# Optimization experiments

Measured on AMD Instinct MI355X. Metric: run time of the kernel, lower is better.

The kernel has to match this reference:

```python
import jax, jax.numpy as jnp
import numpy as np

B, L, D_BERT, D_PROJ, N_SPANS, HIDDEN, EXTRA = 128, 512, 1024, 64, 3, 512, 17
BN_EPS = 1e-5


def setup_inputs() -> dict:
    key = jax.random.key(0)
    ks = jax.random.split(key, 20)
    inp = {
        "bert_outputs": jax.random.normal(ks[0], (B, L, D_BERT), jnp.float32),
        "offsets": jnp.sort(jax.random.randint(ks[1], (B, N_SPANS, 2), 0, L), axis=-1),
        "in_urls": jax.random.uniform(ks[2], (B, 3), jnp.float32),
        "other_feats": jax.random.normal(ks[3], (B, 14), jnp.float32),
        # context conv (Conv1d: out=64, in=1024, k=3)
        "conv_w": jax.random.normal(ks[4], (D_PROJ, D_BERT, 3), jnp.float32) * 0.02,
        "conv_b": jnp.zeros((D_PROJ,), jnp.float32),
        # span extractor global attention Linear(64 -> 1)
        "att_w": jax.random.normal(ks[5], (D_PROJ,), jnp.float32) * 0.1,
        "att_b": jnp.zeros((), jnp.float32),
        # BatchNorm1d(192) in eval mode (running stats)
        "bn1_g": jnp.ones((D_PROJ * 3,), jnp.float32),
        "bn1_b": jnp.zeros((D_PROJ * 3,), jnp.float32),
        "bn1_m": jax.random.normal(ks[6], (D_PROJ * 3,), jnp.float32) * 0.1,
        "bn1_v": jax.random.uniform(ks[7], (D_PROJ * 3,), jnp.float32, 0.5, 1.5),
        # Linear(192 -> 512), kaiming
        "fc_w": jax.random.normal(ks[8], (HIDDEN, D_PROJ * 3), jnp.float32) * np.sqrt(2.0 / (D_PROJ * 3)),
        "fc_b": jnp.zeros((HIDDEN,), jnp.float32),
        # BatchNorm1d(512)
        "bn2_g": jnp.ones((HIDDEN,), jnp.float32),
        "bn2_b": jnp.zeros((HIDDEN,), jnp.float32),
        "bn2_m": jax.random.normal(ks[9], (HIDDEN,), jnp.float32) * 0.1,
        "bn2_v": jax.random.uniform(ks[10], (HIDDEN,), jnp.float32, 0.5, 1.5),
        # new_last_layer Linear(512+17 -> 3)
        "last_w": jax.random.normal(ks[11], (3, HIDDEN + EXTRA), jnp.float32) * 0.05,
        "last_b": jnp.zeros((3,), jnp.float32),
    }
    return inp


def _bn_eval(x, g, b, m, v):
    return (x - m) * jax.lax.rsqrt(v + BN_EPS) * g + b


def reference(bert_outputs, offsets, in_urls, other_feats, conv_w, conv_b,
              att_w, att_b, bn1_g, bn1_b, bn1_m, bn1_v, fc_w, fc_b,
              bn2_g, bn2_b, bn2_m, bn2_v, last_w, last_b):
    # Conv1d over sequence: [B,L,Dbert] -> [B,L,64], padding preserves length
    x = jnp.transpose(bert_outputs, (0, 2, 1))                      # [B, C_in, L]
    conv = jax.lax.conv_general_dilated(
        x, conv_w, window_strides=(1,), padding=[(1, 1)],
        dimension_numbers=("NCH", "OIH", "NCH"))
    conv = jnp.transpose(conv + conv_b[None, :, None], (0, 2, 1))   # [B, L, 64]

    # SelfAttentiveSpanExtractor: per-token logits, masked softmax within span, weighted sum
    logits = jnp.einsum("bld,d->bl", conv, att_w) + att_b           # [B, L]
    pos = jnp.arange(L)
    starts = offsets[..., 0][..., None]                             # [B, S, 1]
    ends = offsets[..., 1][..., None]
    span_mask = (pos[None, None, :] >= starts) & (pos[None, None, :] <= ends)  # [B,S,L]
    masked_logits = jnp.where(span_mask, logits[:, None, :], -1e9)
    attn = jax.nn.softmax(masked_logits, axis=-1)                   # [B, S, L]
    span_emb = jnp.einsum("bsl,bld->bsd", attn, conv)               # [B, S, 64]
    extracted = span_emb.reshape(span_emb.shape[0], -1)             # [B, 192]

    # fc: BN -> Linear -> ReLU -> BN -> Dropout(eval=identity)
    h = _bn_eval(extracted, bn1_g, bn1_b, bn1_m, bn1_v)
    h = jax.nn.relu(h @ fc_w.T + fc_b)
    h = _bn_eval(h, bn2_g, bn2_b, bn2_m, bn2_v)

    cat = jnp.concatenate([h, in_urls, other_feats], axis=1)        # [B, 529]
    return cat @ last_w.T + last_b                                  # [B, 3]
```

## Files before the change

kernel.cpp:

```cpp
#include <hip/hip_runtime.h>


typedef _Float16 f16x8 __attribute__((ext_vector_type(8)));
typedef _Float16 f16x4 __attribute__((ext_vector_type(4)));
typedef float    f32x4 __attribute__((ext_vector_type(4)));

#define B_      128
#define L_      512
#define DBERT   1024
#define DPROJ   64
#define NSPANS  3
#define HIDDEN  512
#define KSTEPS  32
#define BM      64
#define AROWS   66
#define ASTR    1032

__global__ __launch_bounds__(256)
void pack_w_kernel(const float* __restrict__ Wc, _Float16* __restrict__ Bp) {
    int idx = blockIdx.x * 256 + threadIdx.x;
    if (idx >= 32 * 3 * 4 * 64) return;
    int lane = idx & 63;
    int rest = idx >> 6;
    int nf   = rest & 3;
    int r2   = rest >> 2;
    int t    = r2 % 3;
    int kb   = r2 / 3;
    int o     = nf * 16 + (lane & 15);
    int kbase = kb * 32 + ((lane >> 4) << 3);
    f16x8 v;
    #pragma unroll
    for (int j = 0; j < 8; ++j)
        v[j] = (_Float16)Wc[(size_t)o * (DBERT * 3) + (size_t)(kbase + j) * 3 + t];
    *(f16x8*)(Bp + (size_t)idx * 8) = v;
}

__global__ __launch_bounds__(512, 2)
void conv_gemm_kernel(const float* __restrict__ X, const _Float16* __restrict__ Bp,
                      const float* __restrict__ cb, const float* __restrict__ aw,
                      const float* __restrict__ ab_p,
                      float* __restrict__ Y, float* __restrict__ Lg) {
    __shared__ __align__(16) _Float16 As[AROWS * ASTR];
    __shared__ __align__(16) _Float16 Bs[2][6144];
    __shared__ float loglds[4][BM];

    const int tid  = threadIdx.x;
    const int wv   = tid >> 6;
    const int lane = tid & 63;
    const int m0   = blockIdx.x * BM;
    const int l0   = m0 & (L_ - 1);
    const int g0   = m0 - l0;

    {
        float4 v[9];
        #pragma unroll
        for (int c = 0; c < 8; ++c) {
            int s = tid + c * 512;
            int r = s >> 7, off = s & 127;
            int l = l0 - 1 + r;
            v[c] = make_float4(0.f, 0.f, 0.f, 0.f);
            if (l >= 0 && l < L_)
                v[c] = *(const float4*)(X + (size_t)(g0 + l) * DBERT + off * 4);
        }
        #pragma unroll
        for (int c = 0; c < 8; ++c) {
            int s = tid + c * 512;
            int r = s >> 7, off = s & 127;
            f16x4 h = {(_Float16)v[c].x, (_Float16)v[c].y, (_Float16)v[c].z, (_Float16)v[c].w};
            *(f16x4*)(&As[r * ASTR + off * 4]) = h;
        }
        #pragma unroll
        for (int c = 8; c < 17; ++c) {
            bool act = (c < 16) || (tid < 256);
            int s = tid + c * 512;
            int r = s >> 7, off = s & 127;
            int l = l0 - 1 + r;
            v[c - 8] = make_float4(0.f, 0.f, 0.f, 0.f);
            if (act && l >= 0 && l < L_)
                v[c - 8] = *(const float4*)(X + (size_t)(g0 + l) * DBERT + off * 4);
        }
        #pragma unroll
        for (int c = 8; c < 17; ++c) {
            bool act = (c < 16) || (tid < 256);
            if (act) {
                int s = tid + c * 512;
                int r = s >> 7, off = s & 127;
                f16x4 h = {(_Float16)v[c - 8].x, (_Float16)v[c - 8].y,
                           (_Float16)v[c - 8].z, (_Float16)v[c - 8].w};
                *(f16x4*)(&As[r * ASTR + off * 4]) = h;
            }
        }
        const uint4* bsrc = (const uint4*)Bp;
        uint4* bdst = (uint4*)&Bs[0][0];
        bdst[tid] = bsrc[tid];
        if (tid < 256) bdst[512 + tid] = bsrc[512 + tid];
    }
    __syncthreads();

    const f32x4 vzero = {0.f, 0.f, 0.f, 0.f};
    f32x4 acc[2];
    acc[0] = vzero; acc[1] = vzero;

    const int mrow0 = (wv & 1) * 32;
    const int ch    = wv >> 1;

    float4 vaq[2][2];

    #pragma unroll 2
    for (int kb = 0; kb < KSTEPS; ++kb) {
        const int p = kb & 1;

        if (kb >= 2 && kb <= 10) {
            #pragma unroll
            for (int j = 0; j < 2; ++j) {
                int c = 2 * (kb - 2) + j;
                if (c < 16 || (c == 16 && tid < 256)) {
                    int s = 512 * c + tid;
                    int r = s >> 7, off = s & 127;
                    float4 v = vaq[p][j];
                    f16x4 h = {(_Float16)v.x, (_Float16)v.y, (_Float16)v.z, (_Float16)v.w};
                    *(f16x4*)(&As[r * ASTR + 512 + off * 4]) = h;
                }
            }
        }
        uint4 vb0, vb1;
        const bool haveB = (kb + 1) < KSTEPS;
        if (haveB) {
            const uint4* bsrc = (const uint4*)(Bp + (size_t)(kb + 1) * 6144);
            vb0 = bsrc[tid];
            if (tid < 256) vb1 = bsrc[512 + tid];
        }
        if (kb <= 8) {
            #pragma unroll
            for (int j = 0; j < 2; ++j) {
                int c = 2 * kb + j;
                if (c < 16 || (c == 16 && tid < 256)) {
                    int s = 512 * c + tid;
                    int r = s >> 7, off = s & 127;
                    int l = l0 - 1 + r;
                    float4 v = make_float4(0.f, 0.f, 0.f, 0.f);
                    if (l >= 0 && l < L_)
                        v = *(const float4*)(X + (size_t)(g0 + l) * DBERT + 512 + off * 4);
                    vaq[p][j] = v;
                }
            }
        }

        f16x8 afr[2][3], bfr[3];
        #pragma unroll
        for (int mf = 0; mf < 2; ++mf)
            #pragma unroll
            for (int t = 0; t < 3; ++t)
                afr[mf][t] = *(const f16x8*)(
                    &As[(mrow0 + mf * 16 + (lane & 15) + t) * ASTR + kb * 32 + ((lane >> 4) << 3)]);
        #pragma unroll
        for (int t = 0; t < 3; ++t)
            bfr[t] = *(const f16x8*)(&Bs[p][(((t * 4 + ch) * 64) + lane) * 8]);
        #pragma unroll
        for (int mf = 0; mf < 2; ++mf)
            #pragma unroll
            for (int t = 0; t < 3; ++t)
                acc[mf] = __builtin_amdgcn_mfma_f32_16x16x32_f16(
                    afr[mf][t], bfr[t], acc[mf], 0, 0, 0);

        if (haveB) {
            uint4* bdst = (uint4*)&Bs[p ^ 1][0];
            bdst[tid] = vb0;
            if (tid < 256) bdst[512 + tid] = vb1;
        }
        __syncthreads();
    }

    const float awl = aw[ch * 16 + (lane & 15)];
    #pragma unroll
    for (int mf = 0; mf < 2; ++mf) {
        int col = ch * 16 + (lane & 15);
        float bias = cb[col];
        #pragma unroll
        for (int i = 0; i < 4; ++i) {
            int row = m0 + mrow0 + mf * 16 + ((lane >> 4) << 2) + i;
            Y[(size_t)row * DPROJ + col] = acc[mf][i] + bias;
        }
        #pragma unroll
        for (int i = 0; i < 4; ++i) {
            float pl = acc[mf][i] * awl;
            pl += __shfl_xor(pl, 1); pl += __shfl_xor(pl, 2);
            pl += __shfl_xor(pl, 4); pl += __shfl_xor(pl, 8);
            if ((lane & 15) == 0)
                loglds[ch][mrow0 + mf * 16 + ((lane >> 4) << 2) + i] = pl;
        }
    }
    __syncthreads();
    if (tid < BM) {
        float bdot = 0.f;
        #pragma unroll 16
        for (int c = 0; c < DPROJ; ++c) bdot += cb[c] * aw[c];
        Lg[m0 + tid] = loglds[0][tid] + loglds[1][tid] + loglds[2][tid] + loglds[3][tid]
                       + bdot + ab_p[0];
    }
}

__global__ __launch_bounds__(256)
void span_emb_kernel(const float* __restrict__ conv, const float* __restrict__ Lg,
                     const int* __restrict__ offs, float* __restrict__ emb) {
    __shared__ float logits[L_];
    __shared__ float red[8];
    __shared__ float part[256];

    const int bs   = blockIdx.x;
    const int b    = bs / NSPANS;
    const int sp   = bs - b * NSPANS;
    const int tid  = threadIdx.x;
    const int lane = tid & 63;
    const int wv   = tid >> 6;

    if (tid < 128)
        *(float4*)(&logits[tid * 4]) = *(const float4*)(Lg + (size_t)b * L_ + tid * 4);
    __syncthreads();

    const int st = offs[b * (NSPANS * 2) + sp * 2 + 0];
    const int en = offs[b * (NSPANS * 2) + sp * 2 + 1];

    float mx = -1e30f;
    for (int l = st + tid; l <= en; l += 256) mx = fmaxf(mx, logits[l]);
    #pragma unroll
    for (int off = 32; off >= 1; off >>= 1) mx = fmaxf(mx, __shfl_xor(mx, off));
    if (lane == 0) red[wv] = mx;
    __syncthreads();
    mx = fmaxf(fmaxf(red[0], red[1]), fmaxf(red[2], red[3]));
    __syncthreads();

    float sm = 0.f;
    for (int l = st + tid; l <= en; l += 256) sm += __expf(logits[l] - mx);
    #pragma unroll
    for (int off = 32; off >= 1; off >>= 1) sm += __shfl_xor(sm, off);
    if (lane == 0) red[wv] = sm;
    __syncthreads();
    const float denom = red[0] + red[1] + red[2] + red[3];

    float a = 0.f;
    for (int l = st + wv; l <= en; l += 4)
        a += __expf(logits[l] - mx) * conv[((size_t)b * L_ + l) * DPROJ + lane];
    part[tid] = a;
    __syncthreads();
    if (tid < DPROJ)
        emb[(size_t)bs * DPROJ + tid] =
            (part[tid] + part[64 + tid] + part[128 + tid] + part[192 + tid]) / denom;
}

__global__ __launch_bounds__(256)
void span_fc_kernel(const float* __restrict__ emb_in,
                    const float* __restrict__ in_urls, const float* __restrict__ other,
                    const float* __restrict__ bn1_g, const float* __restrict__ bn1_b,
                    const float* __restrict__ bn1_m, const float* __restrict__ bn1_v,
                    const float* __restrict__ fc_w, const float* __restrict__ fc_b,
                    const float* __restrict__ bn2_g, const float* __restrict__ bn2_b,
                    const float* __restrict__ bn2_m, const float* __restrict__ bn2_v,
                    const float* __restrict__ last_w, const float* __restrict__ last_b,
                    float* __restrict__ out) {
    __shared__ float emb[NSPANS * DPROJ];
    __shared__ float hbuf[HIDDEN];

    const int b    = blockIdx.x;
    const int tid  = threadIdx.x;
    const int lane = tid & 63;
    const int wv   = tid >> 6;

    if (tid < NSPANS * DPROJ) {
        float e = emb_in[(size_t)b * (NSPANS * DPROJ) + tid];
        emb[tid] = (e - bn1_m[tid]) * rsqrtf(bn1_v[tid] + 1e-5f) * bn1_g[tid] + bn1_b[tid];
    }
    __syncthreads();

    #pragma unroll
    for (int q = 0; q < 2; ++q) {
        const int j = tid + q * 256;
        const float* wrow = fc_w + (size_t)j * (NSPANS * DPROJ);
        float s = fc_b[j];
        #pragma unroll 8
        for (int i = 0; i < NSPANS * DPROJ; ++i) s += wrow[i] * emb[i];
        s = fmaxf(s, 0.f);
        hbuf[j] = (s - bn2_m[j]) * rsqrtf(bn2_v[j] + 1e-5f) * bn2_g[j] + bn2_b[j];
    }
    __syncthreads();

    if (wv < 3) {
        const float* lw = last_w + wv * (HIDDEN + 17);
        float s = 0.f;
        for (int i = lane; i < HIDDEN + 17; i += 64) {
            float f;
            if (i < HIDDEN)          f = hbuf[i];
            else if (i < HIDDEN + 3) f = in_urls[b * 3 + (i - HIDDEN)];
            else                     f = other[b * 14 + (i - HIDDEN - 3)];
            s += lw[i] * f;
        }
        #pragma unroll
        for (int off = 32; off >= 1; off >>= 1) s += __shfl_xor(s, off);
        if (lane == 0) out[b * 3 + wv] = s + last_b[wv];
    }
}

extern "C" void kernel_launch(void* const* d_in, const int* in_sizes, int n_in,
                              void* d_out, int out_size, void* d_ws, size_t ws_size,
                              hipStream_t stream) {
    const float* bert    = (const float*)d_in[0];
    const int*   offs    = (const int*)d_in[1];
    const float* in_urls = (const float*)d_in[2];
    const float* other   = (const float*)d_in[3];
    const float* conv_w  = (const float*)d_in[4];
    const float* conv_b  = (const float*)d_in[5];
    const float* att_w   = (const float*)d_in[6];
    const float* att_b   = (const float*)d_in[7];
    const float* bn1_g   = (const float*)d_in[8];
    const float* bn1_b   = (const float*)d_in[9];
    const float* bn1_m   = (const float*)d_in[10];
    const float* bn1_v   = (const float*)d_in[11];
    const float* fc_w    = (const float*)d_in[12];
    const float* fc_b    = (const float*)d_in[13];
    const float* bn2_g   = (const float*)d_in[14];
    const float* bn2_b   = (const float*)d_in[15];
    const float* bn2_m   = (const float*)d_in[16];
    const float* bn2_v   = (const float*)d_in[17];
    const float* last_w  = (const float*)d_in[18];
    const float* last_b  = (const float*)d_in[19];

    _Float16* Bp      = (_Float16*)d_ws;
    float*    convout = (float*)((char*)d_ws + 393216);
    float*    logits  = (float*)((char*)d_ws + 393216 + (size_t)B_ * L_ * DPROJ * 4);
    float*    emb     = (float*)((char*)d_ws + 393216 + (size_t)B_ * L_ * DPROJ * 4 + 262144);

    hipLaunchKernelGGL(pack_w_kernel, dim3(96), dim3(256), 0, stream, conv_w, Bp);
    hipLaunchKernelGGL(conv_gemm_kernel, dim3((B_ * L_) / BM), dim3(512), 0, stream,
                       bert, Bp, conv_b, att_w, att_b, convout, logits);
    hipLaunchKernelGGL(span_emb_kernel, dim3(B_ * NSPANS), dim3(256), 0, stream,
                       convout, logits, offs, emb);
    hipLaunchKernelGGL(span_fc_kernel, dim3(B_), dim3(256), 0, stream,
                       emb, in_urls, other,
                       bn1_g, bn1_b, bn1_m, bn1_v, fc_w, fc_b,
                       bn2_g, bn2_b, bn2_m, bn2_v, last_w, last_b,
                       (float*)d_out);
}
```

Baseline: 166.7 us.

## Restructure conv GEMM to 32-row tiles with 32x32 MFMA and split-K waves

Halves the row tile to 32 and uses 256-thread blocks. The conv GEMM moves from 16x16x32 to 32x32x16 MFMA, with two waves splitting K and reducing through LDS. B fragments now load straight from global into registers with one-step prefetch, replacing the double-buffered shared B and per-step barriers. A is loaded fully up front instead of half being pipelined. This removes the K-loop barriers and LDS B traffic and doubles the grid. The costs are more halo-row overhead (34 rows loaded for every 32), an up-front load stall, and repeated global reads of B per block.

```diff
diff --git a/kernel.cpp b/kernel.cpp
--- a/kernel.cpp
+++ b/kernel.cpp
@@ -3,7 +3,7 @@
 
 typedef _Float16 f16x8 __attribute__((ext_vector_type(8)));
 typedef _Float16 f16x4 __attribute__((ext_vector_type(4)));
-typedef float    f32x4 __attribute__((ext_vector_type(4)));
+typedef float    f32x16 __attribute__((ext_vector_type(16)));
 
 #define B_      128
 #define L_      512
@@ -12,22 +12,22 @@
 #define NSPANS  3
 #define HIDDEN  512
 #define KSTEPS  32
-#define BM      64
-#define AROWS   66
+#define BM      32
+#define AROWS   34
 #define ASTR    1032
 
 __global__ __launch_bounds__(256)
 void pack_w_kernel(const float* __restrict__ Wc, _Float16* __restrict__ Bp) {
     int idx = blockIdx.x * 256 + threadIdx.x;
-    if (idx >= 32 * 3 * 4 * 64) return;
+    if (idx >= 384 * 64) return;
     int lane = idx & 63;
-    int rest = idx >> 6;
-    int nf   = rest & 3;
-    int r2   = rest >> 2;
-    int t    = r2 % 3;
-    int kb   = r2 / 3;
-    int o     = nf * 16 + (lane & 15);
-    int kbase = kb * 32 + ((lane >> 4) << 3);
+    int f    = idx >> 6;
+    int ch   = f & 1;
+    int ks   = (f >> 1) & 1;
+    int t    = (f >> 2) % 3;
+    int kb   = (f >> 2) / 3;
+    int o     = ch * 32 + (lane & 31);
+    int kbase = kb * 32 + ks * 16 + ((lane >> 5) << 3);
     f16x8 v;
     #pragma unroll
     for (int j = 0; j < 8; ++j)
@@ -35,169 +35,102 @@
     *(f16x8*)(Bp + (size_t)idx * 8) = v;
 }
 
-__global__ __launch_bounds__(512, 2)
+__global__ __launch_bounds__(256, 2)
 void conv_gemm_kernel(const float* __restrict__ X, const _Float16* __restrict__ Bp,
                       const float* __restrict__ cb, const float* __restrict__ aw,
                       const float* __restrict__ ab_p,
                       float* __restrict__ Y, float* __restrict__ Lg) {
-    __shared__ __align__(16) _Float16 As[AROWS * ASTR];
-    __shared__ __align__(16) _Float16 Bs[2][6144];
-    __shared__ float loglds[4][BM];
+    __shared__ __align__(16) char shraw[AROWS * ASTR * 2];
+    __shared__ float loglds[2][BM];
+
+    _Float16* As = (_Float16*)shraw;
 
     const int tid  = threadIdx.x;
     const int wv   = tid >> 6;
     const int lane = tid & 63;
+    const int ch   = wv & 1;
+    const int ks   = wv >> 1;
     const int m0   = blockIdx.x * BM;
     const int l0   = m0 & (L_ - 1);
     const int g0   = m0 - l0;
 
-    {
-        float4 v[9];
-        #pragma unroll
-        for (int c = 0; c < 8; ++c) {
-            int s = tid + c * 512;
-            int r = s >> 7, off = s & 127;
-            int l = l0 - 1 + r;
-            v[c] = make_float4(0.f, 0.f, 0.f, 0.f);
-            if (l >= 0 && l < L_)
-                v[c] = *(const float4*)(X + (size_t)(g0 + l) * DBERT + off * 4);
-        }
-        #pragma unroll
-        for (int c = 0; c < 8; ++c) {
-            int s = tid + c * 512;
-            int r = s >> 7, off = s & 127;
-            f16x4 h = {(_Float16)v[c].x, (_Float16)v[c].y, (_Float16)v[c].z, (_Float16)v[c].w};
-            *(f16x4*)(&As[r * ASTR + off * 4]) = h;
-        }
-        #pragma unroll
-        for (int c = 8; c < 17; ++c) {
-            bool act = (c < 16) || (tid < 256);
-            int s = tid + c * 512;
-            int r = s >> 7, off = s & 127;
-            int l = l0 - 1 + r;
-            v[c - 8] = make_float4(0.f, 0.f, 0.f, 0.f);
-            if (act && l >= 0 && l < L_)
-                v[c - 8] = *(const float4*)(X + (size_t)(g0 + l) * DBERT + off * 4);
-        }
-        #pragma unroll
-        for (int c = 8; c < 17; ++c) {
-            bool act = (c < 16) || (tid < 256);
-            if (act) {
-                int s = tid + c * 512;
-                int r = s >> 7, off = s & 127;
-                f16x4 h = {(_Float16)v[c - 8].x, (_Float16)v[c - 8].y,
-                           (_Float16)v[c - 8].z, (_Float16)v[c - 8].w};
-                *(f16x4*)(&As[r * ASTR + off * 4]) = h;
+    f16x8 bcur[3], bnxt[3];
+    #pragma unroll
+    for (int t = 0; t < 3; ++t)
+        bcur[t] = *(const f16x8*)(Bp + ((size_t)((t * 2 + ks) * 2 + ch) * 64 + lane) * 8);
+
+    #pragma unroll
+    for (int base = 0; base < 34; base += 8) {
+        const int n = (base + 8 <= 34) ? 8 : (34 - base);
+        float4 v[8];
+        #pragma unroll
+        for (int i = 0; i < 8; ++i) {
+            if (i < n) {
+                int l = l0 - 1 + base + i;
+                v[i] = make_float4(0.f, 0.f, 0.f, 0.f);
+                if (l >= 0 && l < L_)
+                    v[i] = *(const float4*)(X + (size_t)(g0 + l) * DBERT + tid * 4);
             }
         }
-        const uint4* bsrc = (const uint4*)Bp;
-        uint4* bdst = (uint4*)&Bs[0][0];
-        bdst[tid] = bsrc[tid];
-        if (tid < 256) bdst[512 + tid] = bsrc[512 + tid];
-    }
-    __syncthreads();
-
-    const f32x4 vzero = {0.f, 0.f, 0.f, 0.f};
-    f32x4 acc[2];
-    acc[0] = vzero; acc[1] = vzero;
-
-    const int mrow0 = (wv & 1) * 32;
-    const int ch    = wv >> 1;
-
-    float4 vaq[2][2];
-
+        #pragma unroll
+        for (int i = 0; i < 8; ++i) {
+            if (i < n) {
+                f16x4 h = {(_Float16)v[i].x, (_Float16)v[i].y,
+                           (_Float16)v[i].z, (_Float16)v[i].w};
+                *(f16x4*)(&As[(base + i) * ASTR + tid * 4]) = h;
+            }
+        }
+    }
+    __syncthreads();
+
+    f32x16 acc = {};
     #pragma unroll 2
     for (int kb = 0; kb < KSTEPS; ++kb) {
-        const int p = kb & 1;
-
-        if (kb >= 2 && kb <= 10) {
-            #pragma unroll
-            for (int j = 0; j < 2; ++j) {
-                int c = 2 * (kb - 2) + j;
-                if (c < 16 || (c == 16 && tid < 256)) {
-                    int s = 512 * c + tid;
-                    int r = s >> 7, off = s & 127;
-                    float4 v = vaq[p][j];
-                    f16x4 h = {(_Float16)v.x, (_Float16)v.y, (_Float16)v.z, (_Float16)v.w};
-                    *(f16x4*)(&As[r * ASTR + 512 + off * 4]) = h;
-                }
-            }
-        }
-        uint4 vb0, vb1;
-        const bool haveB = (kb + 1) < KSTEPS;
-        if (haveB) {
-            const uint4* bsrc = (const uint4*)(Bp + (size_t)(kb + 1) * 6144);
-            vb0 = bsrc[tid];
-            if (tid < 256) vb1 = bsrc[512 + tid];
-        }
-        if (kb <= 8) {
-            #pragma unroll
-            for (int j = 0; j < 2; ++j) {
-                int c = 2 * kb + j;
-                if (c < 16 || (c == 16 && tid < 256)) {
-                    int s = 512 * c + tid;
-                    int r = s >> 7, off = s & 127;
-                    int l = l0 - 1 + r;
-                    float4 v = make_float4(0.f, 0.f, 0.f, 0.f);
-                    if (l >= 0 && l < L_)
-                        v = *(const float4*)(X + (size_t)(g0 + l) * DBERT + 512 + off * 4);
-                    vaq[p][j] = v;
-                }
-            }
-        }
-
-        f16x8 afr[2][3], bfr[3];
-        #pragma unroll
-        for (int mf = 0; mf < 2; ++mf)
+        if (kb + 1 < KSTEPS) {
             #pragma unroll
             for (int t = 0; t < 3; ++t)
-                afr[mf][t] = *(const f16x8*)(
-                    &As[(mrow0 + mf * 16 + (lane & 15) + t) * ASTR + kb * 32 + ((lane >> 4) << 3)]);
+                bnxt[t] = *(const f16x8*)(
+                    Bp + ((size_t)((((kb + 1) * 3 + t) * 2 + ks) * 2 + ch) * 64 + lane) * 8);
+        }
+        f16x8 afr[3];
+        const int kboff = kb * 32 + ks * 16 + ((lane >> 5) << 3);
         #pragma unroll
         for (int t = 0; t < 3; ++t)
-            bfr[t] = *(const f16x8*)(&Bs[p][(((t * 4 + ch) * 64) + lane) * 8]);
-        #pragma unroll
-        for (int mf = 0; mf < 2; ++mf)
-            #pragma unroll
-            for (int t = 0; t < 3; ++t)
-                acc[mf] = __builtin_amdgcn_mfma_f32_16x16x32_f16(
-                    afr[mf][t], bfr[t], acc[mf], 0, 0, 0);
-
-        if (haveB) {
-            uint4* bdst = (uint4*)&Bs[p ^ 1][0];
-            bdst[tid] = vb0;
-            if (tid < 256) bdst[512 + tid] = vb1;
-        }
-        __syncthreads();
-    }
-
-    const float awl = aw[ch * 16 + (lane & 15)];
-    #pragma unroll
-    for (int mf = 0; mf < 2; ++mf) {
-        int col = ch * 16 + (lane & 15);
-        float bias = cb[col];
-        #pragma unroll
-        for (int i = 0; i < 4; ++i) {
-            int row = m0 + mrow0 + mf * 16 + ((lane >> 4) << 2) + i;
-            Y[(size_t)row * DPROJ + col] = acc[mf][i] + bias;
-        }
-        #pragma unroll
-        for (int i = 0; i < 4; ++i) {
-            float pl = acc[mf][i] * awl;
-            pl += __shfl_xor(pl, 1); pl += __shfl_xor(pl, 2);
-            pl += __shfl_xor(pl, 4); pl += __shfl_xor(pl, 8);
-            if ((lane & 15) == 0)
-                loglds[ch][mrow0 + mf * 16 + ((lane >> 4) << 2) + i] = pl;
-        }
-    }
-    __syncthreads();
-    if (tid < BM) {
-        float bdot = 0.f;
-        #pragma unroll 16
-        for (int c = 0; c < DPROJ; ++c) bdot += cb[c] * aw[c];
-        Lg[m0 + tid] = loglds[0][tid] + loglds[1][tid] + loglds[2][tid] + loglds[3][tid]
-                       + bdot + ab_p[0];
-    }
+            afr[t] = *(const f16x8*)(&As[((lane & 31) + t) * ASTR + kboff]);
+        #pragma unroll
+        for (int t = 0; t < 3; ++t)
+            acc = __builtin_amdgcn_mfma_f32_32x32x16_f16(afr[t], bcur[t], acc, 0, 0, 0);
+        #pragma unroll
+        for (int t = 0; t < 3; ++t) bcur[t] = bnxt[t];
+    }
+
+    __syncthreads();
+    float* red = (float*)shraw;
+    if (ks == 1) {
+        #pragma unroll
+        for (int i = 0; i < 16; ++i) red[(ch * 64 + lane) * 16 + i] = acc[i];
+    }
+    __syncthreads();
+    if (ks == 0) {
+        const int col = ch * 32 + (lane & 31);
+        const float cbv = cb[col];
+        const float awv = aw[col];
+        const int rbase = (lane >> 5) << 2;
+        #pragma unroll
+        for (int i = 0; i < 16; ++i) {
+            float c = acc[i] + red[(ch * 64 + lane) * 16 + i] + cbv;
+            int row = (i & 3) + 8 * (i >> 2) + rbase;
+            Y[(size_t)(m0 + row) * DPROJ + col] = c;
+            float p = c * awv;
+            p += __shfl_xor(p, 1);  p += __shfl_xor(p, 2);
+            p += __shfl_xor(p, 4);  p += __shfl_xor(p, 8);
+            p += __shfl_xor(p, 16);
+            if ((lane & 31) == 0) loglds[ch][row] = p;
+        }
+    }
+    __syncthreads();
+    if (tid < BM)
+        Lg[m0 + tid] = loglds[0][tid] + loglds[1][tid] + ab_p[0];
 }
 
 __global__ __launch_bounds__(256)
@@ -330,7 +263,7 @@
     float*    emb     = (float*)((char*)d_ws + 393216 + (size_t)B_ * L_ * DPROJ * 4 + 262144);
 
     hipLaunchKernelGGL(pack_w_kernel, dim3(96), dim3(256), 0, stream, conv_w, Bp);
-    hipLaunchKernelGGL(conv_gemm_kernel, dim3((B_ * L_) / BM), dim3(512), 0, stream,
+    hipLaunchKernelGGL(conv_gemm_kernel, dim3((B_ * L_) / BM), dim3(256), 0, stream,
                        bert, Bp, conv_b, att_w, att_b, convout, logits);
     hipLaunchKernelGGL(span_emb_kernel, dim3(B_ * NSPANS), dim3(256), 0, stream,
                        convout, logits, offs, emb);
```

Result: faster. 152.1 us (-8.8%).
